# Kernel tuning notes

Hardware: AMD Instinct MI355X
Metric: run time of the kernel (lower is better)

Reference implementation:

```python
import jax, jax.numpy as jnp
import numpy as np

B = 4096       # batch size
DIM = 1024     # feature dim
E = 9          # 8 session experts + 1 default layer (index 8)


def setup_inputs() -> dict:
    key = jax.random.key(0)
    k_x, k_w, k_b, k_i = jax.random.split(key, 4)
    x = jax.random.normal(k_x, (B, DIM), dtype=jnp.float32)
    # Stacked nn.Linear params: W[e] has torch layout [out, in], b[e] is [out].
    # (Original init is identity+zero bias; random values exercise the same math.)
    W = jax.random.normal(k_w, (E, DIM, DIM), dtype=jnp.float32) * (DIM ** -0.5)
    b = jax.random.normal(k_b, (E, DIM), dtype=jnp.float32)
    session_idx = jax.random.randint(k_i, (B,), 0, E, dtype=jnp.int64)
    return {"x": x, "W": W, "b": b, "session_idx": session_idx}


def reference(x, W, b, session_idx):
    # Per-sample keyed linear: out[i] = x[i] @ W[session_idx[i]].T + b[session_idx[i]].
    # Dense formulation: run every expert on every sample (E small), then select.
    # y: [B, E, DIM]
    y = jnp.einsum('bd,eod->beo', x, W) + b[None, :, :]
    out = y[jnp.arange(x.shape[0]), session_idx]  # [B, DIM]
    return out
```

## Files before the change

### kernel.cpp

```cpp
#include <hip/hip_runtime.h>
#include <hip/hip_bf16.h>

#define NE 9
#define NDIM 1024
#define BM 64
#define BN 128
#define BK 64
#define NT (NDIM / BK)
#define MAX_SLOTS 80

typedef __attribute__((ext_vector_type(8))) short bf16x8;
typedef __attribute__((ext_vector_type(4))) float f32x4;

__device__ __forceinline__ unsigned pack2_bf16(float a, float b) {
    __hip_bfloat162 h = __float22bfloat162_rn(float2{a, b});
    return *reinterpret_cast<unsigned*>(&h);
}

__device__ __forceinline__ void gload_lds16(const void* g, void* l) {
    __builtin_amdgcn_global_load_lds(
        (const __attribute__((address_space(1))) unsigned int*)g,
        (__attribute__((address_space(3))) unsigned int*)l, 16, 0, 0);
}

__global__ __launch_bounds__(256)
void prep_kernel(const float* __restrict__ x, const float* __restrict__ W,
                 const int* __restrict__ sidx,
                 unsigned short* __restrict__ xb, unsigned short* __restrict__ Wb,
                 int* __restrict__ perm, int* __restrict__ offsets,
                 int* __restrict__ slot_e, int* __restrict__ slot_m0,
                 int* __restrict__ nslots, int nB) {
    if (blockIdx.x == 0) {
        __shared__ int cnt[NE];
        __shared__ int cur[NE];
        int t = threadIdx.x;
        if (t < NE) cnt[t] = 0;
        __syncthreads();
        for (int i = t; i < nB; i += 256) atomicAdd(&cnt[sidx[i]], 1);
        __syncthreads();
        if (t == 0) {
            int run = 0, s = 0;
            for (int e = 0; e < NE; ++e) {
                cur[e] = run; offsets[e] = run;
                for (int m0 = 0; m0 < cnt[e]; m0 += BM) {
                    slot_e[s] = e; slot_m0[s] = m0; ++s;
                }
                run += cnt[e];
            }
            offsets[NE] = run;
            *nslots = s;
        }
        __syncthreads();
        for (int i = t; i < nB; i += 256) {
            int p = atomicAdd(&cur[sidx[i]], 1);
            perm[p] = i;
        }
    } else {
        const int NW8 = NE * NDIM * (NDIM / 8);
        const int NX8 = nB * (NDIM / 8);
        const int tot = NW8 + NX8;
        const int stride = (gridDim.x - 1) * 256;
        for (int u = (blockIdx.x - 1) * 256 + threadIdx.x; u < tot; u += stride) {
            const float4* src;
            uint4* dst;
            if (u < NW8) {
                src = (const float4*)W + 2 * (size_t)u;
                dst = (uint4*)Wb + u;
            } else {
                size_t v = (size_t)(u - NW8);
                src = (const float4*)x + 2 * v;
                dst = (uint4*)xb + v;
            }
            float4 a = src[0], c = src[1];
            uint4 o;
            o.x = pack2_bf16(a.x, a.y);
            o.y = pack2_bf16(a.z, a.w);
            o.z = pack2_bf16(c.x, c.y);
            o.w = pack2_bf16(c.z, c.w);
            *dst = o;
        }
    }
}

__global__ __launch_bounds__(256, 2)
void gemm_bf16_kernel(const unsigned short* __restrict__ xb,
                      const unsigned short* __restrict__ Wb,
                      const float* __restrict__ bias,
                      const int* __restrict__ perm,
                      const int* __restrict__ offsets,
                      const int* __restrict__ slot_e,
                      const int* __restrict__ slot_m0,
                      const int* __restrict__ nslots,
                      float* __restrict__ out) {
    const int b    = blockIdx.x;
    const int xcd  = b & 7;
    const int j    = b >> 3;
    const int ns   = *nslots;
    const int q    = ns >> 3, r = ns & 7;
    const int mine = q + (xcd < r ? 1 : 0);
    const int ls   = j >> 3;
    if (ls >= mine) return;
    const int slot = xcd * q + (xcd < r ? xcd : r) + ls;
    const int n    = j & 7;

    const int e   = slot_e[slot];
    const int m0  = slot_m0[slot];
    const int off = offsets[e];
    const int cnt = offsets[e + 1] - off;
    const int n0  = n * BN;

    __shared__ __align__(16) unsigned short lds[36864];

    const int t    = threadIdx.x;
    const int wave = t >> 6;
    const int lane = t & 63;
    const int fr   = lane & 15;
    const int fq   = lane >> 4;
    const int wr   = (wave >> 1) * 32;
    const int wc   = (wave & 1) * 64;
    const int xr   = fr & 7;

    const int srow = t >> 3;
    const int scol = ((t & 7) ^ (srow & 7)) * 8;
    int lm0 = m0 + srow;      if (lm0 >= cnt) lm0 = cnt - 1;
    int lm1 = m0 + 32 + srow; if (lm1 >= cnt) lm1 = cnt - 1;
    const unsigned short* asrc0 = xb + (size_t)perm[off + lm0] * NDIM + scol;
    const unsigned short* asrc1 = xb + (size_t)perm[off + lm1] * NDIM + scol;
    const unsigned short* bsrc  = Wb + ((size_t)e * NDIM + n0 + srow) * NDIM + scol;

#define STAGE(BUF, K0)                                                         \
    do {                                                                       \
        const int _ab = (BUF) * 4096;                                          \
        const int _bb = 12288 + (BUF) * 8192;                                  \
        gload_lds16(asrc0 + (K0), &lds[_ab + wave * 512]);                     \
        gload_lds16(asrc1 + (K0), &lds[_ab + 2048 + wave * 512]);              \
        _Pragma("unroll")                                                      \
        for (int i = 0; i < 4; ++i)                                            \
            gload_lds16(bsrc + (size_t)i * 32 * NDIM + (K0),                   \
                        &lds[_bb + i * 2048 + wave * 512]);                    \
    } while (0)

    f32x4 acc[2][4];
#pragma unroll
    for (int i = 0; i < 2; ++i)
#pragma unroll
        for (int k = 0; k < 4; ++k) acc[i][k] = (f32x4)(0.0f);

    STAGE(0, 0);
    STAGE(1, BK);
    asm volatile("s_waitcnt vmcnt(6)" ::: "memory");
    __builtin_amdgcn_s_barrier();

    int cur = 0;
#pragma unroll
    for (int tt = 0; tt < NT; ++tt) {
        if (tt + 2 < NT) {
            int sb = cur + 2; if (sb >= 3) sb -= 3;
            STAGE(sb, (tt + 2) * BK);
        }

        const int abase = cur * 4096;
        const int bbase = 12288 + cur * 8192;
#pragma unroll
        for (int kk = 0; kk < 2; ++kk) {
            const int cs = ((kk * 4 + fq) ^ xr) * 8;
            bf16x8 af[2], bfv[4];
#pragma unroll
            for (int mf = 0; mf < 2; ++mf)
                af[mf] = *reinterpret_cast<const bf16x8*>(
                    &lds[abase + (wr + mf * 16 + fr) * 64 + cs]);
#pragma unroll
            for (int nf = 0; nf < 4; ++nf)
                bfv[nf] = *reinterpret_cast<const bf16x8*>(
                    &lds[bbase + (wc + nf * 16 + fr) * 64 + cs]);
#pragma unroll
            for (int mf = 0; mf < 2; ++mf)
#pragma unroll
                for (int nf = 0; nf < 4; ++nf)
                    acc[mf][nf] = __builtin_amdgcn_mfma_f32_16x16x32_bf16(
                        af[mf], bfv[nf], acc[mf][nf], 0, 0, 0);
        }

        if (tt + 1 < NT) {
            if (tt + 2 < NT)
                asm volatile("s_waitcnt vmcnt(6)" ::: "memory");
            else
                asm volatile("s_waitcnt vmcnt(0)" ::: "memory");
            __builtin_amdgcn_s_barrier();
        }
        cur = (cur + 1 < 3) ? cur + 1 : 0;
    }
#undef STAGE

    float bl[4];
#pragma unroll
    for (int nf = 0; nf < 4; ++nf)
        bl[nf] = bias[e * NDIM + n0 + wc + nf * 16 + fr];

#pragma unroll
    for (int mf = 0; mf < 2; ++mf) {
#pragma unroll
        for (int jr = 0; jr < 4; ++jr) {
            int lm = wr + mf * 16 + fq * 4 + jr;
            if (m0 + lm < cnt) {
                int grow = perm[off + m0 + lm];
                float* orow = out + (size_t)grow * NDIM;
#pragma unroll
                for (int nf = 0; nf < 4; ++nf)
                    orow[n0 + wc + nf * 16 + fr] = acc[mf][nf][jr] + bl[nf];
            }
        }
    }
}

__global__ void naive_kernel(const float* __restrict__ x, const float* __restrict__ W,
                             const float* __restrict__ bias,
                             const int* __restrict__ sidx, float* __restrict__ out,
                             int nB) {
    int i = blockIdx.x;
    int c = threadIdx.x + (blockIdx.y << 8);
    if (i >= nB || c >= NDIM) return;
    int e = sidx[i];
    const float* w = W + ((size_t)e * NDIM + c) * NDIM;
    const float* xr = x + (size_t)i * NDIM;
    float s = bias[e * NDIM + c];
    for (int k = 0; k < NDIM; ++k) s += xr[k] * w[k];
    out[(size_t)i * NDIM + c] = s;
}

extern "C" void kernel_launch(void* const* d_in, const int* in_sizes, int n_in,
                              void* d_out, int out_size, void* d_ws, size_t ws_size,
                              hipStream_t stream) {
    const float* x    = (const float*)d_in[0];
    const float* W    = (const float*)d_in[1];
    const float* bias = (const float*)d_in[2];
    const int*   sidx = (const int*)d_in[3];
    float*       out  = (float*)d_out;

    const int nB = in_sizes[3];

    char* wsb = (char*)d_ws;
    size_t p_off   = (size_t)nB * 4;
    size_t p_slote = p_off + 64;
    size_t p_slotm = p_slote + MAX_SLOTS * 4;
    size_t p_nslot = p_slotm + MAX_SLOTS * 4;
    size_t p_xb    = ((p_nslot + 4 + 511) / 512) * 512;
    size_t p_wb    = p_xb + (size_t)nB * NDIM * 2;
    size_t need    = p_wb + (size_t)NE * NDIM * NDIM * 2;

    if (ws_size < need) {
        dim3 g(nB, NDIM / 256);
        naive_kernel<<<g, 256, 0, stream>>>(x, W, bias, sidx, out, nB);
        return;
    }

    int* perm    = (int*)(wsb + 0);
    int* offsets = (int*)(wsb + p_off);
    int* slot_e  = (int*)(wsb + p_slote);
    int* slot_m0 = (int*)(wsb + p_slotm);
    int* nslots  = (int*)(wsb + p_nslot);
    unsigned short* xb = (unsigned short*)(wsb + p_xb);
    unsigned short* Wb = (unsigned short*)(wsb + p_wb);

    prep_kernel<<<1024, 256, 0, stream>>>(x, W, sidx, xb, Wb, perm, offsets,
                                          slot_e, slot_m0, nslots, nB);

    gemm_bf16_kernel<<<MAX_SLOTS * 8, 256, 0, stream>>>(
        xb, Wb, bias, perm, offsets, slot_e, slot_m0, nslots, out);
}
```

Baseline: 44.02 us.

## Fuse x bf16 conversion into GEMM A-load and shrink N tile

The prep kernel no longer converts x to bf16. The GEMM now loads fp32 rows of x through registers, converts them and writes them to LDS with a double-buffered register prefetch, which removes the xb round trip through global memory. The N tile is halved to 64 with a 4-blocks-per-CU launch bound and a fixed grid of 72x16 slots using a precomputed descriptor array, giving more blocks for load balance. The trade-off is that each block re-reads and re-converts fp32 x, and W is reloaded for twice as many tiles, with a two-stage rather than three-stage pipeline.

After: 52.45 us. 1.19x slower.

```diff
diff --git a/kernel.cpp b/kernel.cpp
--- a/kernel.cpp
+++ b/kernel.cpp
@@ -4,10 +4,11 @@
 #define NE 9
 #define NDIM 1024
 #define BM 64
-#define BN 128
+#define BN 64
 #define BK 64
 #define NT (NDIM / BK)
-#define MAX_SLOTS 80
+#define NSLOT_MAX 72
+#define WPX 144
 
 typedef __attribute__((ext_vector_type(8))) short bf16x8;
 typedef __attribute__((ext_vector_type(4))) float f32x4;
@@ -24,12 +25,9 @@
 }
 
 __global__ __launch_bounds__(256)
-void prep_kernel(const float* __restrict__ x, const float* __restrict__ W,
-                 const int* __restrict__ sidx,
-                 unsigned short* __restrict__ xb, unsigned short* __restrict__ Wb,
-                 int* __restrict__ perm, int* __restrict__ offsets,
-                 int* __restrict__ slot_e, int* __restrict__ slot_m0,
-                 int* __restrict__ nslots, int nB) {
+void prep_kernel(const float* __restrict__ W, const int* __restrict__ sidx,
+                 unsigned short* __restrict__ Wb,
+                 int* __restrict__ perm, int4* __restrict__ desc, int nB) {
     if (blockIdx.x == 0) {
         __shared__ int cnt[NE];
         __shared__ int cur[NE];
@@ -41,14 +39,15 @@
         if (t == 0) {
             int run = 0, s = 0;
             for (int e = 0; e < NE; ++e) {
-                cur[e] = run; offsets[e] = run;
-                for (int m0 = 0; m0 < cnt[e]; m0 += BM) {
-                    slot_e[s] = e; slot_m0[s] = m0; ++s;
+                cur[e] = run;
+                int c = cnt[e];
+                for (int m0 = 0; m0 < c; m0 += BM) {
+                    desc[s] = make_int4(e, run + m0, min(BM, c - m0), 0);
+                    ++s;
                 }
-                run += cnt[e];
+                run += c;
             }
-            offsets[NE] = run;
-            *nslots = s;
+            for (; s < NSLOT_MAX; ++s) desc[s] = make_int4(-1, 0, 1, 0);
         }
         __syncthreads();
         for (int i = t; i < nB; i += 256) {
@@ -57,59 +56,37 @@
         }
     } else {
         const int NW8 = NE * NDIM * (NDIM / 8);
-        const int NX8 = nB * (NDIM / 8);
-        const int tot = NW8 + NX8;
         const int stride = (gridDim.x - 1) * 256;
-        for (int u = (blockIdx.x - 1) * 256 + threadIdx.x; u < tot; u += stride) {
-            const float4* src;
-            uint4* dst;
-            if (u < NW8) {
-                src = (const float4*)W + 2 * (size_t)u;
-                dst = (uint4*)Wb + u;
-            } else {
-                size_t v = (size_t)(u - NW8);
-                src = (const float4*)x + 2 * v;
-                dst = (uint4*)xb + v;
-            }
+        for (int u = (blockIdx.x - 1) * 256 + threadIdx.x; u < NW8; u += stride) {
+            const float4* src = (const float4*)W + 2 * (size_t)u;
             float4 a = src[0], c = src[1];
             uint4 o;
             o.x = pack2_bf16(a.x, a.y);
             o.y = pack2_bf16(a.z, a.w);
             o.z = pack2_bf16(c.x, c.y);
             o.w = pack2_bf16(c.z, c.w);
-            *dst = o;
-        }
-    }
-}
-
-__global__ __launch_bounds__(256, 2)
-void gemm_bf16_kernel(const unsigned short* __restrict__ xb,
-                      const unsigned short* __restrict__ Wb,
-                      const float* __restrict__ bias,
-                      const int* __restrict__ perm,
-                      const int* __restrict__ offsets,
-                      const int* __restrict__ slot_e,
-                      const int* __restrict__ slot_m0,
-                      const int* __restrict__ nslots,
-                      float* __restrict__ out) {
+            ((uint4*)Wb)[u] = o;
+        }
+    }
+}
+
+__global__ __launch_bounds__(256, 4)
+void gemm_kernel(const float* __restrict__ x,
+                 const unsigned short* __restrict__ Wb,
+                 const float* __restrict__ bias,
+                 const int* __restrict__ perm,
+                 const int4* __restrict__ desc,
+                 float* __restrict__ out) {
     const int b    = blockIdx.x;
-    const int xcd  = b & 7;
-    const int j    = b >> 3;
-    const int ns   = *nslots;
-    const int q    = ns >> 3, r = ns & 7;
-    const int mine = q + (xcd < r ? 1 : 0);
-    const int ls   = j >> 3;
-    if (ls >= mine) return;
-    const int slot = xcd * q + (xcd < r ? xcd : r) + ls;
-    const int n    = j & 7;
-
-    const int e   = slot_e[slot];
-    const int m0  = slot_m0[slot];
-    const int off = offsets[e];
-    const int cnt = offsets[e + 1] - off;
-    const int n0  = n * BN;
-
-    __shared__ __align__(16) unsigned short lds[36864];
+    const int w    = (b & 7) * WPX + (b >> 3);
+    const int slot = w >> 4;
+    const int n    = w & 15;
+    const int4 d   = desc[slot];
+    if (d.x < 0) return;
+    const int e = d.x, rowstart = d.y, rcnt = d.z;
+    const int n0 = n * BN;
+
+    __shared__ __align__(16) unsigned short lds[16384];
 
     const int t    = threadIdx.x;
     const int wave = t >> 6;
@@ -117,84 +94,103 @@
     const int fr   = lane & 15;
     const int fq   = lane >> 4;
     const int wr   = (wave >> 1) * 32;
-    const int wc   = (wave & 1) * 64;
+    const int wc   = (wave & 1) * 32;
     const int xr   = fr & 7;
 
     const int srow = t >> 3;
-    const int scol = ((t & 7) ^ (srow & 7)) * 8;
-    int lm0 = m0 + srow;      if (lm0 >= cnt) lm0 = cnt - 1;
-    int lm1 = m0 + 32 + srow; if (lm1 >= cnt) lm1 = cnt - 1;
-    const unsigned short* asrc0 = xb + (size_t)perm[off + lm0] * NDIM + scol;
-    const unsigned short* asrc1 = xb + (size_t)perm[off + lm1] * NDIM + scol;
-    const unsigned short* bsrc  = Wb + ((size_t)e * NDIM + n0 + srow) * NDIM + scol;
-
-#define STAGE(BUF, K0)                                                         \
+    const int c8   = t & 7;
+    const int sc   = c8 ^ (srow & 7);
+
+    int lm0 = srow;      if (lm0 >= rcnt) lm0 = rcnt - 1;
+    int lm1 = srow + 32; if (lm1 >= rcnt) lm1 = rcnt - 1;
+    const float* ap0 = x + (size_t)perm[rowstart + lm0] * NDIM + c8 * 8;
+    const float* ap1 = x + (size_t)perm[rowstart + lm1] * NDIM + c8 * 8;
+    const unsigned short* bp =
+        Wb + ((size_t)e * NDIM + n0 + srow) * NDIM + sc * 8;
+
+    float4 av[4];
+
+#define LOADA(K0)                                                              \
     do {                                                                       \
-        const int _ab = (BUF) * 4096;                                          \
-        const int _bb = 12288 + (BUF) * 8192;                                  \
-        gload_lds16(asrc0 + (K0), &lds[_ab + wave * 512]);                     \
-        gload_lds16(asrc1 + (K0), &lds[_ab + 2048 + wave * 512]);              \
-        _Pragma("unroll")                                                      \
-        for (int i = 0; i < 4; ++i)                                            \
-            gload_lds16(bsrc + (size_t)i * 32 * NDIM + (K0),                   \
-                        &lds[_bb + i * 2048 + wave * 512]);                    \
+        av[0] = *(const float4*)(ap0 + (K0));                                  \
+        av[1] = *(const float4*)(ap0 + (K0) + 4);                              \
+        av[2] = *(const float4*)(ap1 + (K0));                                  \
+        av[3] = *(const float4*)(ap1 + (K0) + 4);                              \
     } while (0)
 
-    f32x4 acc[2][4];
+#define CVTA(BUF)                                                              \
+    do {                                                                       \
+        uint4 o0, o1;                                                          \
+        o0.x = pack2_bf16(av[0].x, av[0].y);                                   \
+        o0.y = pack2_bf16(av[0].z, av[0].w);                                   \
+        o0.z = pack2_bf16(av[1].x, av[1].y);                                   \
+        o0.w = pack2_bf16(av[1].z, av[1].w);                                   \
+        o1.x = pack2_bf16(av[2].x, av[2].y);                                   \
+        o1.y = pack2_bf16(av[2].z, av[2].w);                                   \
+        o1.z = pack2_bf16(av[3].x, av[3].y);                                   \
+        o1.w = pack2_bf16(av[3].z, av[3].w);                                   \
+        *reinterpret_cast<uint4*>(&lds[(BUF) * 4096 + srow * 64 + sc * 8]) = o0;      \
+        *reinterpret_cast<uint4*>(&lds[(BUF) * 4096 + (srow + 32) * 64 + sc * 8]) = o1;\
+    } while (0)
+
+#define STAGEB(BUF, K0)                                                        \
+    do {                                                                       \
+        gload_lds16(bp + (K0), &lds[8192 + (BUF) * 4096 + wave * 512]);        \
+        gload_lds16(bp + (size_t)32 * NDIM + (K0),                             \
+                    &lds[8192 + (BUF) * 4096 + 2048 + wave * 512]);            \
+    } while (0)
+
+    f32x4 acc[2][2];
 #pragma unroll
     for (int i = 0; i < 2; ++i)
 #pragma unroll
-        for (int k = 0; k < 4; ++k) acc[i][k] = (f32x4)(0.0f);
-
-    STAGE(0, 0);
-    STAGE(1, BK);
-    asm volatile("s_waitcnt vmcnt(6)" ::: "memory");
-    __builtin_amdgcn_s_barrier();
-
-    int cur = 0;
-#pragma unroll
+        for (int k = 0; k < 2; ++k) acc[i][k] = (f32x4)(0.0f);
+
+    LOADA(0);
+    STAGEB(0, 0);
+    CVTA(0);
+    LOADA(BK);
+    __syncthreads();
+
     for (int tt = 0; tt < NT; ++tt) {
-        if (tt + 2 < NT) {
-            int sb = cur + 2; if (sb >= 3) sb -= 3;
-            STAGE(sb, (tt + 2) * BK);
-        }
+        const int cur = tt & 1;
+        if (tt + 1 < NT) STAGEB(cur ^ 1, (tt + 1) * BK);
 
         const int abase = cur * 4096;
-        const int bbase = 12288 + cur * 8192;
+        const int bbase = 8192 + cur * 4096;
 #pragma unroll
         for (int kk = 0; kk < 2; ++kk) {
             const int cs = ((kk * 4 + fq) ^ xr) * 8;
-            bf16x8 af[2], bfv[4];
+            bf16x8 af[2], bfv[2];
 #pragma unroll
             for (int mf = 0; mf < 2; ++mf)
                 af[mf] = *reinterpret_cast<const bf16x8*>(
                     &lds[abase + (wr + mf * 16 + fr) * 64 + cs]);
 #pragma unroll
-            for (int nf = 0; nf < 4; ++nf)
+            for (int nf = 0; nf < 2; ++nf)
                 bfv[nf] = *reinterpret_cast<const bf16x8*>(
                     &lds[bbase + (wc + nf * 16 + fr) * 64 + cs]);
 #pragma unroll
             for (int mf = 0; mf < 2; ++mf)
 #pragma unroll
-                for (int nf = 0; nf < 4; ++nf)
+                for (int nf = 0; nf < 2; ++nf)
                     acc[mf][nf] = __builtin_amdgcn_mfma_f32_16x16x32_bf16(
                         af[mf], bfv[nf], acc[mf][nf], 0, 0, 0);
         }
 
         if (tt + 1 < NT) {
-            if (tt + 2 < NT)
-                asm volatile("s_waitcnt vmcnt(6)" ::: "memory");
-            else
-                asm volatile("s_waitcnt vmcnt(0)" ::: "memory");
-            __builtin_amdgcn_s_barrier();
-        }
-        cur = (cur + 1 < 3) ? cur + 1 : 0;
-    }
-#undef STAGE
-
-    float bl[4];
-#pragma unroll
-    for (int nf = 0; nf < 4; ++nf)
+            CVTA(cur ^ 1);
+            if (tt + 2 < NT) LOADA((tt + 2) * BK);
+            __syncthreads();
+        }
+    }
+#undef LOADA
+#undef CVTA
+#undef STAGEB
+
+    float bl[2];
+#pragma unroll
+    for (int nf = 0; nf < 2; ++nf)
         bl[nf] = bias[e * NDIM + n0 + wc + nf * 16 + fr];
 
 #pragma unroll
@@ -202,11 +198,11 @@
 #pragma unroll
         for (int jr = 0; jr < 4; ++jr) {
             int lm = wr + mf * 16 + fq * 4 + jr;
-            if (m0 + lm < cnt) {
-                int grow = perm[off + m0 + lm];
+            if (lm < rcnt) {
+                int grow = perm[rowstart + lm];
                 float* orow = out + (size_t)grow * NDIM;
 #pragma unroll
-                for (int nf = 0; nf < 4; ++nf)
+                for (int nf = 0; nf < 2; ++nf)
                     orow[n0 + wc + nf * 16 + fr] = acc[mf][nf][jr] + bl[nf];
             }
         }
@@ -221,10 +217,10 @@
     int c = threadIdx.x + (blockIdx.y << 8);
     if (i >= nB || c >= NDIM) return;
     int e = sidx[i];
-    const float* w = W + ((size_t)e * NDIM + c) * NDIM;
+    const float* wrow = W + ((size_t)e * NDIM + c) * NDIM;
     const float* xr = x + (size_t)i * NDIM;
     float s = bias[e * NDIM + c];
-    for (int k = 0; k < NDIM; ++k) s += xr[k] * w[k];
+    for (int k = 0; k < NDIM; ++k) s += xr[k] * wrow[k];
     out[(size_t)i * NDIM + c] = s;
 }
 
@@ -240,13 +236,9 @@
     const int nB = in_sizes[3];
 
     char* wsb = (char*)d_ws;
-    size_t p_off   = (size_t)nB * 4;
-    size_t p_slote = p_off + 64;
-    size_t p_slotm = p_slote + MAX_SLOTS * 4;
-    size_t p_nslot = p_slotm + MAX_SLOTS * 4;
-    size_t p_xb    = ((p_nslot + 4 + 511) / 512) * 512;
-    size_t p_wb    = p_xb + (size_t)nB * NDIM * 2;
-    size_t need    = p_wb + (size_t)NE * NDIM * NDIM * 2;
+    size_t p_desc = (size_t)nB * 4;
+    size_t p_wb   = ((p_desc + NSLOT_MAX * 16 + 511) / 512) * 512;
+    size_t need   = p_wb + (size_t)NE * NDIM * NDIM * 2;
 
     if (ws_size < need) {
         dim3 g(nB, NDIM / 256);
@@ -254,17 +246,11 @@
         return;
     }
 
-    int* perm    = (int*)(wsb + 0);
-    int* offsets = (int*)(wsb + p_off);
-    int* slot_e  = (int*)(wsb + p_slote);
-    int* slot_m0 = (int*)(wsb + p_slotm);
-    int* nslots  = (int*)(wsb + p_nslot);
-    unsigned short* xb = (unsigned short*)(wsb + p_xb);
+    int*  perm = (int*)wsb;
+    int4* desc = (int4*)(wsb + p_desc);
     unsigned short* Wb = (unsigned short*)(wsb + p_wb);
 
-    prep_kernel<<<1024, 256, 0, stream>>>(x, W, sidx, xb, Wb, perm, offsets,
-                                          slot_e, slot_m0, nslots, nB);
-
-    gemm_bf16_kernel<<<MAX_SLOTS * 8, 256, 0, stream>>>(
-        xb, Wb, bias, perm, offsets, slot_e, slot_m0, nslots, out);
-}
+    prep_kernel<<<1024, 256, 0, stream>>>(W, sidx, Wb, perm, desc, nB);
+
+    gemm_kernel<<<NSLOT_MAX * 16, 256, 0, stream>>>(x, Wb, bias, perm, desc, out);
+}
```
